# Optimization experiments

Measured on AMD Instinct MI355X. Metric: run time of the kernel, lower is better.

The kernel has to match this reference:

```python
import jax, jax.numpy as jnp
import numpy as np

N_EMBD = 1024
N_HEAD = 16
HEAD_DIM = N_EMBD // N_HEAD


def setup_inputs() -> dict:
    key = jax.random.key(0)
    ks = jax.random.split(key, 9)
    B, T, C = 4, 2048, N_EMBD
    s = 1.0 / np.sqrt(C)
    return {
        "x": jax.random.normal(ks[0], (B, T, C), dtype=jnp.float32),
        "Wk": jax.random.normal(ks[1], (C, C), dtype=jnp.float32) * s,
        "bk": jax.random.normal(ks[2], (C,), dtype=jnp.float32) * 0.02,
        "Wq": jax.random.normal(ks[3], (C, C), dtype=jnp.float32) * s,
        "bq": jax.random.normal(ks[4], (C,), dtype=jnp.float32) * 0.02,
        "Wv": jax.random.normal(ks[5], (C, C), dtype=jnp.float32) * s,
        "bv": jax.random.normal(ks[6], (C,), dtype=jnp.float32) * 0.02,
        "Wp": jax.random.normal(ks[7], (C, C), dtype=jnp.float32) * s,
        "bp": jax.random.normal(ks[8], (C,), dtype=jnp.float32) * 0.02,
    }


def reference(x, Wk, bk, Wq, bq, Wv, bv, Wp, bp):
    B, T, C = x.shape
    nh, hs = N_HEAD, HEAD_DIM
    # linear projections; weights stored as [in, out] (x @ W + b)
    k = (x @ Wk + bk).reshape(B, T, nh, hs).transpose(0, 2, 1, 3)  # [B,nh,T,hs]
    q = (x @ Wq + bq).reshape(B, T, nh, hs).transpose(0, 2, 1, 3)
    v = (x @ Wv + bv).reshape(B, T, nh, hs).transpose(0, 2, 1, 3)
    att = jnp.einsum("bhqd,bhkd->bhqk", q, k) / jnp.sqrt(jnp.float32(hs))
    causal = jnp.tril(jnp.ones((T, T), dtype=bool))  # [T,T]
    att = jnp.where(causal[None, None], att, -jnp.inf)
    att = jax.nn.softmax(att, axis=-1)
    y = jnp.einsum("bhqk,bhkd->bhqd", att, v)  # [B,nh,T,hs]
    y = y.transpose(0, 2, 1, 3).reshape(B, T, C)
    return y @ Wp + bp
```

## Files before the change

### kernel.cpp

```cpp
#include <hip/hip_runtime.h>

#define TSEQ 2048
#define CDIM 1024
#define NH 16
#define HS 64
#define BATCH 4

typedef __attribute__((ext_vector_type(8))) short short8;
typedef __attribute__((ext_vector_type(4))) short s16x4;
typedef __attribute__((ext_vector_type(4))) float f32x4;

__device__ __forceinline__ short f2bf(float f) {
    unsigned u = __builtin_bit_cast(unsigned, f);
    unsigned r = (u + 0x7fffu + ((u >> 16) & 1u)) >> 16;
    return (short)r;
}

__device__ __forceinline__ void gload_lds16(const void* g, void* l) {
    __builtin_amdgcn_global_load_lds((const __attribute__((address_space(1))) void*)g,
                                     (__attribute__((address_space(3))) void*)l, 16, 0, 0);
}

__global__ void cvt_x(const float* __restrict__ x, short* __restrict__ o, int n4) {
    int i = blockIdx.x * 256 + threadIdx.x;
    if (i >= n4) return;
    float4 v = ((const float4*)x)[i];
    s16x4 r;
    r[0] = f2bf(v.x); r[1] = f2bf(v.y); r[2] = f2bf(v.z); r[3] = f2bf(v.w);
    ((s16x4*)o)[i] = r;
}

__global__ void wtrans(const float* __restrict__ Wk, const float* __restrict__ Wq,
                       const float* __restrict__ Wv, const float* __restrict__ Wp,
                       short* __restrict__ Wcat, short* __restrict__ Wpt) {
    const float* src; short* dst;
    if (blockIdx.z == 0)      { src = Wq; dst = Wcat; }
    else if (blockIdx.z == 1) { src = Wk; dst = Wcat + 1048576; }
    else if (blockIdx.z == 2) { src = Wv; dst = Wcat + 2097152; }
    else                      { src = Wp; dst = Wpt; }
    __shared__ float tl[64][65];
    int tx = threadIdx.x & 63, ty = threadIdx.x >> 6;
    int k0 = blockIdx.x * 64, n0 = blockIdx.y * 64;
#pragma unroll
    for (int i = 0; i < 16; ++i) {
        int r = i * 4 + ty;
        tl[r][tx] = src[(size_t)(k0 + r) * CDIM + n0 + tx];
    }
    __syncthreads();
#pragma unroll
    for (int i = 0; i < 16; ++i) {
        int r = i * 4 + ty;
        dst[(size_t)(n0 + r) * CDIM + k0 + tx] = f2bf(tl[tx][r]);
    }
}

__global__ void bias_pack(const float* __restrict__ bq, const float* __restrict__ bk,
                          const float* __restrict__ bv, float* __restrict__ bcat) {
    int i = blockIdx.x * 256 + threadIdx.x;
    if (i < 1024) bcat[i] = bq[i];
    else if (i < 2048) bcat[i] = bk[i - 1024];
    else if (i < 3072) bcat[i] = bv[i - 2048];
}

__global__ __launch_bounds__(512, 4) void gemm96(const short* __restrict__ A,
                                                 const short* __restrict__ Bt,
                                                 const float* __restrict__ bias,
                                                 float alphaQ,
                                                 short* __restrict__ C,
                                                 short* __restrict__ Vt) {
    __shared__ short As[256 * 64];
    __shared__ short Bs[96 * 64];
    const int t = threadIdx.x;
    const int lane = t & 63, w = t >> 6;
    const int lr = lane & 15, lg = lane >> 4;
    const int wr = w >> 1, wc = w & 1;
    const int tl = (blockIdx.x & 7) * 128 + (blockIdx.x >> 3);
    const int mbase = (tl >> 5) * 256, nbase = (tl & 31) * 96;
    f32x4 acc[4][3] = {};
    for (int k0 = 0; k0 < 1024; k0 += 64) {
#pragma unroll
        for (int i = 0; i < 4; ++i) {
            int chunk = i * 512 + t;
            int r = chunk >> 3, c = chunk & 7;
            int cl = c ^ (r & 7);
            gload_lds16(A + (size_t)(mbase + r) * 1024 + k0 + cl * 8, As + chunk * 8);
        }
        {
            int r = t >> 3, c = t & 7;
            int cl = c ^ (r & 7);
            gload_lds16(Bt + (size_t)(nbase + r) * 1024 + k0 + cl * 8, Bs + t * 8);
            if (t < 256) {
                int chunk = 512 + t;
                int r2 = chunk >> 3, c2 = chunk & 7;
                int cl2 = c2 ^ (r2 & 7);
                gload_lds16(Bt + (size_t)(nbase + r2) * 1024 + k0 + cl2 * 8, Bs + chunk * 8);
            }
        }
        __syncthreads();
#pragma unroll
        for (int ks = 0; ks < 2; ++ks) {
            short8 a[4], b[3];
#pragma unroll
            for (int mi = 0; mi < 4; ++mi) {
                int row = wr * 64 + mi * 16 + lr;
                int ch = (ks * 4 + lg) ^ (row & 7);
                a[mi] = *(const short8*)(As + row * 64 + ch * 8);
            }
#pragma unroll
            for (int ni = 0; ni < 3; ++ni) {
                int row = wc * 48 + ni * 16 + lr;
                int ch = (ks * 4 + lg) ^ (row & 7);
                b[ni] = *(const short8*)(Bs + row * 64 + ch * 8);
            }
#pragma unroll
            for (int mi = 0; mi < 4; ++mi)
#pragma unroll
                for (int ni = 0; ni < 3; ++ni)
                    acc[mi][ni] = __builtin_amdgcn_mfma_f32_16x16x32_bf16(a[mi], b[ni],
                                                                          acc[mi][ni], 0, 0, 0);
        }
        __syncthreads();
    }
    const int btok = mbase & (TSEQ - 1);
    const int bidx = mbase >> 11;
#pragma unroll
    for (int mi = 0; mi < 4; ++mi) {
#pragma unroll
        for (int ni = 0; ni < 3; ++ni) {
            const int col = nbase + wc * 48 + ni * 16 + lr;
            const float bv = bias[col];
            if (col >= 2048) {
                const int dfull = col - 2048;
                const int tok0 = btok + wr * 64 + mi * 16 + lg * 4;
                s16x4 pk;
#pragma unroll
                for (int ii = 0; ii < 4; ++ii) pk[ii] = f2bf(acc[mi][ni][ii] + bv);
                *(s16x4*)(Vt + (size_t)(bidx * 1024 + dfull) * TSEQ + tok0) = pk;
            } else {
                const float alpha = (col < 1024) ? alphaQ : 1.0f;
#pragma unroll
                for (int ii = 0; ii < 4; ++ii) {
                    const int row = mbase + wr * 64 + mi * 16 + lg * 4 + ii;
                    C[(size_t)row * 3072 + col] = f2bf((acc[mi][ni][ii] + bv) * alpha);
                }
            }
        }
    }
}

__global__ __launch_bounds__(256) void gemm_bt(const short* __restrict__ A,
                                               const short* __restrict__ Bt,
                                               const float* __restrict__ bias,
                                               float* __restrict__ Cout) {
    __shared__ short As[128 * 64];
    __shared__ short Bs[128 * 64];
    const int t = threadIdx.x;
    const int lane = t & 63, w = t >> 6;
    const int lr = lane & 15, lg = lane >> 4;
    const int wr = w >> 1, wc = w & 1;
    const int mbase = blockIdx.y * 128, nbase = blockIdx.x * 128;
    f32x4 acc[4][4] = {};
    for (int k0 = 0; k0 < 1024; k0 += 64) {
#pragma unroll
        for (int i = 0; i < 4; ++i) {
            int chunk = i * 256 + t;
            int r = chunk >> 3, c = chunk & 7;
            int cl = c ^ (r & 7);
            gload_lds16(A + (size_t)(mbase + r) * 1024 + k0 + cl * 8, As + chunk * 8);
            gload_lds16(Bt + (size_t)(nbase + r) * 1024 + k0 + cl * 8, Bs + chunk * 8);
        }
        __syncthreads();
#pragma unroll
        for (int ks = 0; ks < 2; ++ks) {
            short8 a[4], b[4];
#pragma unroll
            for (int mi = 0; mi < 4; ++mi) {
                int row = wr * 64 + mi * 16 + lr;
                int ch = (ks * 4 + lg) ^ (row & 7);
                a[mi] = *(const short8*)(As + row * 64 + ch * 8);
            }
#pragma unroll
            for (int ni = 0; ni < 4; ++ni) {
                int row = wc * 64 + ni * 16 + lr;
                int ch = (ks * 4 + lg) ^ (row & 7);
                b[ni] = *(const short8*)(Bs + row * 64 + ch * 8);
            }
#pragma unroll
            for (int mi = 0; mi < 4; ++mi)
#pragma unroll
                for (int ni = 0; ni < 4; ++ni)
                    acc[mi][ni] = __builtin_amdgcn_mfma_f32_16x16x32_bf16(a[mi], b[ni],
                                                                          acc[mi][ni], 0, 0, 0);
        }
        __syncthreads();
    }
#pragma unroll
    for (int mi = 0; mi < 4; ++mi) {
#pragma unroll
        for (int ni = 0; ni < 4; ++ni) {
            int col = nbase + wc * 64 + ni * 16 + lr;
            float bv = bias[col];
#pragma unroll
            for (int i = 0; i < 4; ++i) {
                int row = mbase + wr * 64 + mi * 16 + lg * 4 + i;
                Cout[(size_t)row * 1024 + col] = acc[mi][ni][i] + bv;
            }
        }
    }
}

__global__ __launch_bounds__(256, 4) void attn(const short* __restrict__ QKV,
                                               const short* __restrict__ Vt,
                                               short* __restrict__ Y) {
    __shared__ short Kl[2][64 * 64];
    __shared__ short Vl[2][64 * 64];
    __shared__ short Pl[4][16 * 64];
    const int t = threadIdx.x, lane = t & 63, w = t >> 6;
    const int lr = lane & 15, lg = lane >> 4;
    const int bid = blockIdx.x;
    const int cx = bid & 7, sx = bid >> 3;
    const int bh = cx * 8 + (sx >> 4), pb = sx & 15;
    const int b = bh >> 4, h = bh & 15;
    const size_t rowbase = (size_t)b * TSEQ;
    const float SHIFT2 = 17.31234049f;
    const int sr = t >> 3, sc = t & 7, scl = sc ^ (sr & 7);
    const short* Kg = QKV + 1024 + h * HS;

    const int useg0 = 31 - pb, useg1 = pb;
    for (int sg = 0; sg < 2; ++sg) {
        const int u = sg ? useg1 : useg0;
        const int q0w = u * 64 + w * 16;
        const int niter = u + 1;
        short8 qf[2];
#pragma unroll
        for (int ks = 0; ks < 2; ++ks)
            qf[ks] = *(const short8*)(QKV + (rowbase + q0w + lr) * 3072 + h * HS +
                                      ks * 32 + lg * 8);
        float l_i[4] = {0.f, 0.f, 0.f, 0.f};
        f32x4 o[4] = {};
        gload_lds16(Kg + (rowbase + sr) * 3072 + scl * 8, &Kl[0][t * 8]);
        gload_lds16(Kg + (rowbase + 32 + sr) * 3072 + scl * 8, &Kl[0][(256 + t) * 8]);
        gload_lds16(Vt + (size_t)(bh * 64 + sr) * TSEQ + scl * 8, &Vl[0][t * 8]);
        gload_lds16(Vt + (size_t)(bh * 64 + 32 + sr) * TSEQ + scl * 8, &Vl[0][(256 + t) * 8]);
        __syncthreads();
        int buf = 0;
        for (int jt = 0; jt < niter; ++jt) {
            const int j0 = jt * 64;
            if (jt + 1 < niter) {
                const int j0n = j0 + 64;
                gload_lds16(Kg + (rowbase + j0n + sr) * 3072 + scl * 8, &Kl[buf ^ 1][t * 8]);
                gload_lds16(Kg + (rowbase + j0n + 32 + sr) * 3072 + scl * 8,
                            &Kl[buf ^ 1][(256 + t) * 8]);
                gload_lds16(Vt + (size_t)(bh * 64 + sr) * TSEQ + j0n + scl * 8,
                            &Vl[buf ^ 1][t * 8]);
                gload_lds16(Vt + (size_t)(bh * 64 + 32 + sr) * TSEQ + j0n + scl * 8,
                            &Vl[buf ^ 1][(256 + t) * 8]);
            }
            f32x4 s[4];
            __builtin_amdgcn_s_setprio(1);
#pragma unroll
            for (int nt = 0; nt < 4; ++nt) {
                s[nt] = f32x4{0.f, 0.f, 0.f, 0.f};
#pragma unroll
                for (int ks = 0; ks < 2; ++ks) {
                    short8 kf = *(const short8*)(&Kl[buf][(nt * 16 + lr) * 64 +
                                                          (((ks * 4 + lg) ^ (lr & 7)) * 8)]);
                    s[nt] = __builtin_amdgcn_mfma_f32_16x16x32_bf16(qf[ks], kf, s[nt], 0, 0, 0);
                }
            }
            __builtin_amdgcn_s_setprio(0);
            if (jt == niter - 1) {
#pragma unroll
                for (int nt = 0; nt < 4; ++nt)
#pragma unroll
                    for (int i = 0; i < 4; ++i) {
                        int kv = j0 + nt * 16 + lr;
                        int q = q0w + lg * 4 + i;
                        if (kv > q) s[nt][i] = -__builtin_inff();
                    }
            }
#pragma unroll
            for (int i = 0; i < 4; ++i) {
                const int ql = lg * 4 + i;
                float pt[4];
#pragma unroll
                for (int nt = 0; nt < 4; ++nt) {
                    float p = __builtin_amdgcn_exp2f(s[nt][i] - SHIFT2);
                    unsigned uu = __builtin_bit_cast(unsigned, p);
                    int chv = ((nt * 2 + (lr >> 3)) ^ (ql & 7));
                    Pl[w][ql * 64 + chv * 8 + (lr & 7)] = (short)(uu >> 16);
                    pt[nt] = __builtin_bit_cast(float, uu & 0xffff0000u);
                }
                l_i[i] += (pt[0] + pt[1]) + (pt[2] + pt[3]);
            }
            short8 pf[2];
#pragma unroll
            for (int ks = 0; ks < 2; ++ks)
                pf[ks] = *(const short8*)(&Pl[w][lr * 64 + (((ks * 4 + lg) ^ (lr & 7)) * 8)]);
            __builtin_amdgcn_s_setprio(1);
#pragma unroll
            for (int nd = 0; nd < 4; ++nd)
#pragma unroll
                for (int ks = 0; ks < 2; ++ks) {
                    short8 vf = *(const short8*)(&Vl[buf][(nd * 16 + lr) * 64 +
                                                          (((ks * 4 + lg) ^ (lr & 7)) * 8)]);
                    o[nd] = __builtin_amdgcn_mfma_f32_16x16x32_bf16(pf[ks], vf, o[nd], 0, 0, 0);
                }
            __builtin_amdgcn_s_setprio(0);
            __syncthreads();
            buf ^= 1;
        }
#pragma unroll
        for (int i = 0; i < 4; ++i) {
            float l = l_i[i];
            l += __shfl_xor(l, 1);
            l += __shfl_xor(l, 2);
            l += __shfl_xor(l, 4);
            l += __shfl_xor(l, 8);
            float inv = 1.0f / l;
            int q = q0w + lg * 4 + i;
#pragma unroll
            for (int nd = 0; nd < 4; ++nd)
                Y[(rowbase + q) * 1024 + h * HS + nd * 16 + lr] = f2bf(o[nd][i] * inv);
        }
        __syncthreads();
    }
}

extern "C" void kernel_launch(void* const* d_in, const int* in_sizes, int n_in,
                              void* d_out, int out_size, void* d_ws, size_t ws_size,
                              hipStream_t stream) {
    const float* x  = (const float*)d_in[0];
    const float* Wk = (const float*)d_in[1];
    const float* bk = (const float*)d_in[2];
    const float* Wq = (const float*)d_in[3];
    const float* bq = (const float*)d_in[4];
    const float* Wv = (const float*)d_in[5];
    const float* bv = (const float*)d_in[6];
    const float* Wp = (const float*)d_in[7];
    const float* bp = (const float*)d_in[8];
    float* out = (float*)d_out;
    char* ws = (char*)d_ws;
    const size_t MB = 1024 * 1024;
    short* xb   = (short*)(ws);
    short* Wcat = (short*)(ws + 16 * MB);
    short* Wpt  = (short*)(ws + 22 * MB);
    short* QKVb = (short*)(ws + 24 * MB);
    short* Yb   = xb;
    short* VtT  = (short*)d_out;
    float* bcat = (float*)((char*)d_out + 16 * MB);

    const float alphaQ = 0.125f * 1.44269504088896f;

    cvt_x<<<8192, 256, 0, stream>>>(x, xb, 2097152);
    wtrans<<<dim3(16, 16, 4), 256, 0, stream>>>(Wk, Wq, Wv, Wp, Wcat, Wpt);
    bias_pack<<<12, 256, 0, stream>>>(bq, bk, bv, bcat);
    gemm96<<<1024, 512, 0, stream>>>(xb, Wcat, bcat, alphaQ, QKVb, VtT);
    attn<<<1024, 256, 0, stream>>>(QKVb, VtT, Yb);
    gemm_bt<<<dim3(8, 64), 256, 0, stream>>>(Yb, Wpt, bp, out);
}
```

Baseline: 165.6 us.

## Replace 256x96 QKV GEMM with 128x128 tiles, two N-tiles per block

```diff
diff --git a/kernel.cpp b/kernel.cpp
--- a/kernel.cpp
+++ b/kernel.cpp
@@ -62,89 +62,93 @@
     else if (i < 3072) bcat[i] = bv[i - 2048];
 }
 
-__global__ __launch_bounds__(512, 4) void gemm96(const short* __restrict__ A,
-                                                 const short* __restrict__ Bt,
-                                                 const float* __restrict__ bias,
-                                                 float alphaQ,
-                                                 short* __restrict__ C,
-                                                 short* __restrict__ Vt) {
-    __shared__ short As[256 * 64];
-    __shared__ short Bs[96 * 64];
+__global__ __launch_bounds__(256) void gemm_qkv(const short* __restrict__ A,
+                                                const short* __restrict__ Bt,
+                                                const float* __restrict__ bias,
+                                                float alphaQ,
+                                                short* __restrict__ C,
+                                                short* __restrict__ Vt) {
+    __shared__ short As[128 * 64];
+    __shared__ short Bs[128 * 64];
     const int t = threadIdx.x;
     const int lane = t & 63, w = t >> 6;
     const int lr = lane & 15, lg = lane >> 4;
     const int wr = w >> 1, wc = w & 1;
-    const int tl = (blockIdx.x & 7) * 128 + (blockIdx.x >> 3);
-    const int mbase = (tl >> 5) * 256, nbase = (tl & 31) * 96;
-    f32x4 acc[4][3] = {};
-    for (int k0 = 0; k0 < 1024; k0 += 64) {
-#pragma unroll
-        for (int i = 0; i < 4; ++i) {
-            int chunk = i * 512 + t;
-            int r = chunk >> 3, c = chunk & 7;
-            int cl = c ^ (r & 7);
-            gload_lds16(A + (size_t)(mbase + r) * 1024 + k0 + cl * 8, As + chunk * 8);
-        }
-        {
-            int r = t >> 3, c = t & 7;
-            int cl = c ^ (r & 7);
-            gload_lds16(Bt + (size_t)(nbase + r) * 1024 + k0 + cl * 8, Bs + t * 8);
-            if (t < 256) {
-                int chunk = 512 + t;
-                int r2 = chunk >> 3, c2 = chunk & 7;
-                int cl2 = c2 ^ (r2 & 7);
-                gload_lds16(Bt + (size_t)(nbase + r2) * 1024 + k0 + cl2 * 8, Bs + chunk * 8);
-            }
-        }
-        __syncthreads();
-#pragma unroll
-        for (int ks = 0; ks < 2; ++ks) {
-            short8 a[4], b[3];
+    const int xcd = blockIdx.x & 7, idx = blockIdx.x >> 3;
+    const int mbase = (xcd * 8 + idx / 12) * 128;
+    const int j0 = idx % 12;
+    for (int sub = 0; sub < 2; ++sub) {
+        const int ntile = j0 + sub * 12;
+        const int nbase = ntile * 128;
+        f32x4 acc[4][4] = {};
+        for (int k0 = 0; k0 < 1024; k0 += 64) {
+#pragma unroll
+            for (int i = 0; i < 4; ++i) {
+                int chunk = i * 256 + t;
+                int r = chunk >> 3, c = chunk & 7;
+                int cl = c ^ (r & 7);
+                gload_lds16(A + (size_t)(mbase + r) * 1024 + k0 + cl * 8, As + chunk * 8);
+                gload_lds16(Bt + (size_t)(nbase + r) * 1024 + k0 + cl * 8, Bs + chunk * 8);
+            }
+            __syncthreads();
+#pragma unroll
+            for (int ks = 0; ks < 2; ++ks) {
+                short8 a[4], b[4];
+#pragma unroll
+                for (int mi = 0; mi < 4; ++mi) {
+                    int row = wr * 64 + mi * 16 + lr;
+                    int ch = (ks * 4 + lg) ^ (row & 7);
+                    a[mi] = *(const short8*)(As + row * 64 + ch * 8);
+                }
+#pragma unroll
+                for (int ni = 0; ni < 4; ++ni) {
+                    int row = wc * 64 + ni * 16 + lr;
+                    int ch = (ks * 4 + lg) ^ (row & 7);
+                    b[ni] = *(const short8*)(Bs + row * 64 + ch * 8);
+                }
+#pragma unroll
+                for (int mi = 0; mi < 4; ++mi)
+#pragma unroll
+                    for (int ni = 0; ni < 4; ++ni)
+                        acc[mi][ni] = __builtin_amdgcn_mfma_f32_16x16x32_bf16(a[mi], b[ni],
+                                                                              acc[mi][ni], 0, 0, 0);
+            }
+            __syncthreads();
+        }
+        if (nbase >= 2048) {
+            const int btok = mbase & (TSEQ - 1);
+            const int bidx = mbase >> 11;
 #pragma unroll
             for (int mi = 0; mi < 4; ++mi) {
-                int row = wr * 64 + mi * 16 + lr;
-                int ch = (ks * 4 + lg) ^ (row & 7);
-                a[mi] = *(const short8*)(As + row * 64 + ch * 8);
-            }
-#pragma unroll
-            for (int ni = 0; ni < 3; ++ni) {
-                int row = wc * 48 + ni * 16 + lr;
-                int ch = (ks * 4 + lg) ^ (row & 7);
-                b[ni] = *(const short8*)(Bs + row * 64 + ch * 8);
-            }
-#pragma unroll
-            for (int mi = 0; mi < 4; ++mi)
-#pragma unroll
-                for (int ni = 0; ni < 3; ++ni)
-                    acc[mi][ni] = __builtin_amdgcn_mfma_f32_16x16x32_bf16(a[mi], b[ni],
-                                                                          acc[mi][ni], 0, 0, 0);
-        }
-        __syncthreads();
-    }
-    const int btok = mbase & (TSEQ - 1);
-    const int bidx = mbase >> 11;
-#pragma unroll
-    for (int mi = 0; mi < 4; ++mi) {
-#pragma unroll
-        for (int ni = 0; ni < 3; ++ni) {
-            const int col = nbase + wc * 48 + ni * 16 + lr;
-            const float bv = bias[col];
-            if (col >= 2048) {
-                const int dfull = col - 2048;
-                const int tok0 = btok + wr * 64 + mi * 16 + lg * 4;
-                s16x4 pk;
-#pragma unroll
-                for (int ii = 0; ii < 4; ++ii) pk[ii] = f2bf(acc[mi][ni][ii] + bv);
-                *(s16x4*)(Vt + (size_t)(bidx * 1024 + dfull) * TSEQ + tok0) = pk;
-            } else {
-                const float alpha = (col < 1024) ? alphaQ : 1.0f;
-#pragma unroll
-                for (int ii = 0; ii < 4; ++ii) {
-                    const int row = mbase + wr * 64 + mi * 16 + lg * 4 + ii;
-                    C[(size_t)row * 3072 + col] = f2bf((acc[mi][ni][ii] + bv) * alpha);
-                }
-            }
-        }
+#pragma unroll
+                for (int ni = 0; ni < 4; ++ni) {
+                    const int col = nbase + wc * 64 + ni * 16 + lr;
+                    const int dfull = col - 2048;
+                    const float bv = bias[col];
+                    const int tok0 = btok + wr * 64 + mi * 16 + lg * 4;
+                    s16x4 pk;
+#pragma unroll
+                    for (int ii = 0; ii < 4; ++ii) pk[ii] = f2bf(acc[mi][ni][ii] + bv);
+                    *(s16x4*)(Vt + (size_t)(bidx * 1024 + dfull) * TSEQ + tok0) = pk;
+                }
+            }
+        } else {
+            const float alpha = (nbase < 1024) ? alphaQ : 1.0f;
+#pragma unroll
+            for (int mi = 0; mi < 4; ++mi) {
+#pragma unroll
+                for (int ni = 0; ni < 4; ++ni) {
+                    const int col = nbase + wc * 64 + ni * 16 + lr;
+                    const float bv = bias[col];
+#pragma unroll
+                    for (int ii = 0; ii < 4; ++ii) {
+                        const int row = mbase + wr * 64 + mi * 16 + lg * 4 + ii;
+                        C[(size_t)row * 3072 + col] = f2bf((acc[mi][ni][ii] + bv) * alpha);
+                    }
+                }
+            }
+        }
+        __syncthreads();
     }
 }
 
@@ -355,7 +359,7 @@
     cvt_x<<<8192, 256, 0, stream>>>(x, xb, 2097152);
     wtrans<<<dim3(16, 16, 4), 256, 0, stream>>>(Wk, Wq, Wv, Wp, Wcat, Wpt);
     bias_pack<<<12, 256, 0, stream>>>(bq, bk, bv, bcat);
-    gemm96<<<1024, 512, 0, stream>>>(xb, Wcat, bcat, alphaQ, QKVb, VtT);
+    gemm_qkv<<<768, 256, 0, stream>>>(xb, Wcat, bcat, alphaQ, QKVb, VtT);
     attn<<<1024, 256, 0, stream>>>(QKVb, VtT, Yb);
     gemm_bt<<<dim3(8, 64), 256, 0, stream>>>(Yb, Wpt, bp, out);
 }
```

Result: slower. 226.3 us (+36.7%).
